# Kernel optimization log

Measured on AMD Instinct MI355X. Metric: run time of the kernel, lower is better.

The kernel has to match this reference:

```python
import jax, jax.numpy as jnp
import numpy as np

H = 8
DH = 64  # attention_head_size
HID = 512
NEG = -90000000000.0

def _lin(x, w, b):
    return x @ w + b

def _tfs(x):  # [N, HID] -> [H, N, DH]
    n = x.shape[0]
    return x.reshape(n, H, DH).transpose(1, 0, 2)

def _cross(q, ck, v, cv, mask, dw, db):
    # q: [H,N,DH], ck/cv: [H,M,DH], v: [H,N,DH], mask: [N,M]
    s = jnp.einsum('hnd,hmd->hnm', q, ck)
    s = s * mask[None, :, :] / jnp.sqrt(jnp.asarray(DH, s.dtype))
    s = jnp.where(s == 0.0, NEG, s)  # faithful zero->-inf hack
    p = jax.nn.softmax(s, axis=-1)
    ctx = v + jnp.einsum('hnm,hmd->hnd', p, cv)  # residual add of raw value
    n = ctx.shape[1]
    ctx = ctx.transpose(1, 0, 2).reshape(n, H * DH)
    return _lin(ctx, dw, db)

def setup_inputs() -> dict:
    key = jax.random.key(0)
    ks = jax.random.split(key, 24)
    N1, N2, D1 = 4096, 4096, 300
    d = {}
    d['h_head'] = jax.random.normal(ks[0], (N1, D1), jnp.float32)
    d['h_tail'] = jax.random.normal(ks[1], (N2, HID), jnp.float32)
    d['batch_head'] = jnp.sort(jax.random.randint(ks[2], (N1,), 0, 64))
    d['batch_tail'] = jnp.sort(jax.random.randint(ks[3], (N2,), 0, 64))
    def w(k, i, o):
        return jax.random.normal(k, (i, o), jnp.float32) / np.sqrt(i)
    d['map_w'] = w(ks[4], D1, HID); d['map_b'] = jnp.zeros((HID,), jnp.float32)
    names = ['q1', 'k1', 'v1', 'q2', 'k2', 'v2', 'd1', 'd2']
    for i, nm in enumerate(names):
        d[nm + '_w'] = w(ks[5 + i], HID, HID)
        d[nm + '_b'] = jnp.zeros((HID,), jnp.float32)
    return d

def reference(h_head, h_tail, batch_head, batch_tail,
              map_w, map_b,
              q1_w, q1_b, k1_w, k1_b, v1_w, v1_b,
              q2_w, q2_b, k2_w, k2_b, v2_w, v2_b,
              d1_w, d1_b, d2_w, d2_b):
    hh = _lin(h_head, map_w, map_b)  # n_dim1 != n_dim2 -> map
    q_h = _tfs(_lin(hh, q1_w, q1_b))
    k_h = _tfs(_lin(hh, k1_w, k1_b))
    v_h = _tfs(_lin(hh, v1_w, v1_b))
    q_t = _tfs(_lin(h_tail, q2_w, q2_b))
    k_t = _tfs(_lin(h_tail, k2_w, k2_b))
    v_t = _tfs(_lin(h_tail, v2_w, v2_b))
    mask = (batch_head[:, None] == batch_tail[None, :]).astype(jnp.float32)
    out_head = _cross(q_h, k_t, v_h, v_t, mask, d1_w, d1_b)
    out_tail = _cross(q_t, k_h, v_t, v_h, mask.T, d2_w, d2_b)
    return (out_head, out_tail)
```

## Files before the change

### kernel.cpp

```cpp
#include <hip/hip_runtime.h>
#include <hip/hip_bf16.h>
#include <math.h>


typedef __bf16 bf16x8 __attribute__((ext_vector_type(8)));
typedef float  f32x4  __attribute__((ext_vector_type(4)));

#define HID 512
#define NTOK 4096

#define AS1(p) ((const __attribute__((address_space(1))) void*)(p))
#define AS3(p) ((__attribute__((address_space(3))) void*)(p))

__global__ __launch_bounds__(256) void prep_inputs(
    const float* __restrict__ h_head, const float* __restrict__ h_tail,
    const int* __restrict__ bh, const int* __restrict__ bt,
    __bf16* __restrict__ hh_bf, __bf16* __restrict__ ht_bf,
    int* __restrict__ ranges)
{
    const int q = blockIdx.x, z = blockIdx.z, tid = threadIdx.x;

    if (z == 0) {
        if (q == 0 && tid < 128) {
            int b = tid & 63;
            const int* arr = (tid < 64) ? bh : bt;
            int base = (tid < 64) ? 0 : 128;
            int lo = 0, hi = NTOK;
            while (lo < hi) { int mid = (lo + hi) >> 1; if (arr[mid] < b) lo = mid + 1; else hi = mid; }
            int start = lo;
            lo = 0; hi = NTOK;
            while (lo < hi) { int mid = (lo + hi) >> 1; if (arr[mid] <= b) lo = mid + 1; else hi = mid; }
            ranges[base + b] = start;
            ranges[base + 64 + b] = lo;
        }
        for (int idx = tid; idx < 8 * 40; idx += 256) {
            int r   = q * 8 + idx / 40;
            int col = (idx % 40) * 8;
            bf16x8 v;
            if (col + 8 <= 300) {
                float4 f0 = *(const float4*)&h_head[(size_t)r * 300 + col];
                float4 f1 = *(const float4*)&h_head[(size_t)r * 300 + col + 4];
                v[0]=(__bf16)f0.x; v[1]=(__bf16)f0.y; v[2]=(__bf16)f0.z; v[3]=(__bf16)f0.w;
                v[4]=(__bf16)f1.x; v[5]=(__bf16)f1.y; v[6]=(__bf16)f1.z; v[7]=(__bf16)f1.w;
            } else if (col < 300) {
                float4 f0 = *(const float4*)&h_head[(size_t)r * 300 + col];
                v[0]=(__bf16)f0.x; v[1]=(__bf16)f0.y; v[2]=(__bf16)f0.z; v[3]=(__bf16)f0.w;
                v[4]=(__bf16)0.f; v[5]=(__bf16)0.f; v[6]=(__bf16)0.f; v[7]=(__bf16)0.f;
            } else {
                #pragma unroll
                for (int j = 0; j < 8; ++j) v[j] = (__bf16)0.f;
            }
            *(bf16x8*)&hh_bf[(size_t)r * 320 + col] = v;
        }
    } else {
        for (int idx = tid; idx < 8 * 64; idx += 256) {
            int r   = q * 8 + (idx >> 6);
            int col = (idx & 63) * 8;
            float4 f0 = *(const float4*)&h_tail[(size_t)r * 512 + col];
            float4 f1 = *(const float4*)&h_tail[(size_t)r * 512 + col + 4];
            bf16x8 v;
            v[0]=(__bf16)f0.x; v[1]=(__bf16)f0.y; v[2]=(__bf16)f0.z; v[3]=(__bf16)f0.w;
            v[4]=(__bf16)f1.x; v[5]=(__bf16)f1.y; v[6]=(__bf16)f1.z; v[7]=(__bf16)f1.w;
            *(bf16x8*)&ht_bf[(size_t)r * 512 + col] = v;
        }
    }
}

struct TransJobs {
    const float* src[9];
    __bf16*      dst[9];
    int          K[9];
    int          ldT[9];
};

__global__ __launch_bounds__(256) void transpose_weights(TransJobs tj) {
    const int z = blockIdx.z;
    const float* src = tj.src[z];
    __bf16* dst = tj.dst[z];
    const int K = tj.K[z], ldT = tj.ldT[z];
    const int tk = blockIdx.y * 64;
    const int tn = blockIdx.x * 64;
    if (tk >= ldT) return;

    __shared__ __bf16 T[64][72];
    const int tid = threadIdx.x;
    const int r0 = tid >> 4;
    const int c0 = (tid & 15) * 4;
    #pragma unroll
    for (int i = 0; i < 4; ++i) {
        int k = tk + r0 + i * 16;
        float4 v = (k < K) ? *(const float4*)&src[(size_t)k * 512 + tn + c0]
                           : float4{0.f, 0.f, 0.f, 0.f};
        T[r0 + i * 16][c0 + 0] = (__bf16)v.x;
        T[r0 + i * 16][c0 + 1] = (__bf16)v.y;
        T[r0 + i * 16][c0 + 2] = (__bf16)v.z;
        T[r0 + i * 16][c0 + 3] = (__bf16)v.w;
    }
    __syncthreads();

    const int n  = tid >> 2;
    const int kk = (tid & 3) * 16;
    bf16x8 o0, o1;
    #pragma unroll
    for (int j = 0; j < 8; ++j) { o0[j] = T[kk + j][n]; o1[j] = T[kk + 8 + j][n]; }
    __bf16* dp = dst + (size_t)(tn + n) * ldT + tk + kk;
    *(bf16x8*)dp       = o0;
    *(bf16x8*)(dp + 8) = o1;
}

struct GemmJobs {
    const __bf16* A[4];
    const __bf16* W[4];
    const float*  bias[4];
    void*         C[4];
    int           Kp[4];
};

template <typename TC>
__global__ __launch_bounds__(256) void gemm128(GemmJobs jobs) {
    __shared__ __align__(16) __bf16 As[2][4096];
    __shared__ __align__(16) __bf16 Bs[2][4096];

    const int z = blockIdx.z;
    const __bf16* A    = jobs.A[z];
    const __bf16* W    = jobs.W[z];
    const float*  bias = jobs.bias[z];
    TC*           C    = (TC*)jobs.C[z];
    const int     Kp   = jobs.Kp[z];

    const int tid  = threadIdx.x;
    const int wave = tid >> 6;
    const int lane = tid & 63;
    const int quad = lane >> 4;
    const int l16  = lane & 15;
    const int wy   = wave >> 1;
    const int wx   = wave & 1;
    const int rowBase = blockIdx.y * 128;
    const int colBase = blockIdx.x * 128;

    const int s_row = tid >> 2;
    const int s_kc  = ((tid & 3) ^ ((s_row >> 1) & 3)) * 8;

    const __bf16* gA = A + (size_t)(rowBase + s_row) * Kp + s_kc;
    const __bf16* gB = W + (size_t)(colBase + s_row) * Kp + s_kc;
    const int waveOff = wave * 512;

    f32x4 acc[4][4] = {};
    const int nk = Kp >> 5;

    __builtin_amdgcn_global_load_lds(AS1(gA),                   AS3(&As[0][waveOff]),        16, 0, 0);
    __builtin_amdgcn_global_load_lds(AS1(gA + (size_t)64 * Kp), AS3(&As[0][2048 + waveOff]), 16, 0, 0);
    __builtin_amdgcn_global_load_lds(AS1(gB),                   AS3(&Bs[0][waveOff]),        16, 0, 0);
    __builtin_amdgcn_global_load_lds(AS1(gB + (size_t)64 * Kp), AS3(&Bs[0][2048 + waveOff]), 16, 0, 0);

    for (int i = 0; i < nk; ++i) {
        const int cur = i & 1;
        __syncthreads();

        if (i + 1 < nk) {
            const int kt = (i + 1) * 32;
            const int nx = cur ^ 1;
            __builtin_amdgcn_global_load_lds(AS1(gA + kt),                   AS3(&As[nx][waveOff]),        16, 0, 0);
            __builtin_amdgcn_global_load_lds(AS1(gA + kt + (size_t)64 * Kp), AS3(&As[nx][2048 + waveOff]), 16, 0, 0);
            __builtin_amdgcn_global_load_lds(AS1(gB + kt),                   AS3(&Bs[nx][waveOff]),        16, 0, 0);
            __builtin_amdgcn_global_load_lds(AS1(gB + kt + (size_t)64 * Kp), AS3(&Bs[nx][2048 + waveOff]), 16, 0, 0);
        }

        bf16x8 ar[4], br[4];
        #pragma unroll
        for (int ii = 0; ii < 4; ++ii) {
            const int ra = wy * 64 + ii * 16 + l16;
            ar[ii] = *(const bf16x8*)&As[cur][ra * 32 + ((quad ^ ((ra >> 1) & 3)) << 3)];
        }
        #pragma unroll
        for (int jj = 0; jj < 4; ++jj) {
            const int rb = wx * 64 + jj * 16 + l16;
            br[jj] = *(const bf16x8*)&Bs[cur][rb * 32 + ((quad ^ ((rb >> 1) & 3)) << 3)];
        }
        #pragma unroll
        for (int ii = 0; ii < 4; ++ii)
            #pragma unroll
            for (int jj = 0; jj < 4; ++jj)
                acc[ii][jj] = __builtin_amdgcn_mfma_f32_16x16x32_bf16(ar[ii], br[jj], acc[ii][jj], 0, 0, 0);
    }

    #pragma unroll
    for (int jj = 0; jj < 4; ++jj) {
        int col = colBase + wx * 64 + jj * 16 + l16;
        float bv = bias[col];
        #pragma unroll
        for (int ii = 0; ii < 4; ++ii) {
            #pragma unroll
            for (int r = 0; r < 4; ++r) {
                int row = rowBase + wy * 64 + ii * 16 + quad * 4 + r;
                C[(size_t)row * HID + col] = (TC)(acc[ii][jj][r] + bv);
            }
        }
    }
}

__global__ __launch_bounds__(256) void attn_mfma(
    const __bf16* __restrict__ Q0, const __bf16* __restrict__ K0,
    const __bf16* __restrict__ Vr0, const __bf16* __restrict__ Vc0,
    const __bf16* __restrict__ Q1, const __bf16* __restrict__ K1,
    const __bf16* __restrict__ Vr1, const __bf16* __restrict__ Vc1,
    const int* __restrict__ ranges,
    __bf16* __restrict__ O0, __bf16* __restrict__ O1,
    int Nq, int Nk)
{
    __shared__ __align__(16) __bf16 Qs[64][72];
    __shared__ __align__(16) __bf16 Ks[64][72];
    __shared__ __align__(16) __bf16 Vt[64][72];
    __shared__ __align__(16) __bf16 Ps[64][72];

    const int z = blockIdx.z;
    const __bf16* Q    = z ? Q1 : Q0;
    const __bf16* Kg   = z ? K1 : K0;
    const __bf16* Vres = z ? Vr1 : Vr0;
    const __bf16* Vctx = z ? Vc1 : Vc0;
    __bf16* Out        = z ? O1 : O0;
    const int* qstart  = z ? ranges + 128 : ranges;
    const int* qend    = z ? ranges + 192 : ranges + 64;
    const int* kstart  = z ? ranges       : ranges + 128;
    const int* kend    = z ? ranges + 64  : ranges + 192;

    const int h = blockIdx.x, b = blockIdx.y;
    const int qs = qstart[b], qe = qend[b];
    const int ts = kstart[b], te = kend[b];
    const int nq = qe - qs, nk = te - ts;
    if (nq <= 0) return;

    const int tid  = threadIdx.x;
    const int wave = tid >> 6;
    const int lane = tid & 63;
    const int quad = lane >> 4;
    const int l16  = lane & 15;
    const int srow = tid >> 2;
    const int scol = (tid & 3) * 16;

    if (nk <= 0) {
        float* meanv = (float*)Qs;
        if (tid < 64) {
            float s = 0.f;
            for (int m = 0; m < Nk; ++m)
                s += (float)Vctx[(size_t)m * HID + h * 64 + tid];
            meanv[tid] = s / (float)Nk;
        }
        __syncthreads();
        int d = tid & 63;
        for (int r = qs + (tid >> 6); r < qe; r += 4) {
            size_t off = (size_t)r * HID + h * 64 + d;
            Out[off] = (__bf16)((float)Vres[off] + meanv[d]);
        }
        return;
    }

    for (int qc = 0; qc < nq; qc += 64) {
        __syncthreads();
        {
            int qg = min(qs + qc + srow, Nq - 1);
            const __bf16* src = Q + (size_t)qg * HID + h * 64 + scol;
            *(bf16x8*)&Qs[srow][scol]     = *(const bf16x8*)src;
            *(bf16x8*)&Qs[srow][scol + 8] = *(const bf16x8*)(src + 8);
        }
        __syncthreads();
        bf16x8 aq0 = *(const bf16x8*)&Qs[wave * 16 + l16][quad * 8];
        bf16x8 aq1 = *(const bf16x8*)&Qs[wave * 16 + l16][32 + quad * 8];

        f32x4 O[4] = {};
        float Mx[4], L[4];
        #pragma unroll
        for (int r = 0; r < 4; ++r) { Mx[r] = -__builtin_inff(); L[r] = 0.f; }

        for (int kc = 0; kc < nk; kc += 64) {
            __syncthreads();
            {
                int kg = min(ts + kc + srow, Nk - 1);
                const __bf16* ksrc = Kg + (size_t)kg * HID + h * 64 + scol;
                *(bf16x8*)&Ks[srow][scol]     = *(const bf16x8*)ksrc;
                *(bf16x8*)&Ks[srow][scol + 8] = *(const bf16x8*)(ksrc + 8);
                const __bf16* vsrc = Vctx + (size_t)kg * HID + h * 64 + scol;
                bf16x8 v0 = *(const bf16x8*)vsrc;
                bf16x8 v1 = *(const bf16x8*)(vsrc + 8);
                #pragma unroll
                for (int j = 0; j < 8; ++j) {
                    Vt[scol + j][srow]     = v0[j];
                    Vt[scol + 8 + j][srow] = v1[j];
                }
            }
            __syncthreads();

            f32x4 S[4] = {};
            #pragma unroll
            for (int c = 0; c < 4; ++c) {
                bf16x8 bk0 = *(const bf16x8*)&Ks[c * 16 + l16][quad * 8];
                bf16x8 bk1 = *(const bf16x8*)&Ks[c * 16 + l16][32 + quad * 8];
                S[c] = __builtin_amdgcn_mfma_f32_16x16x32_bf16(aq0, bk0, S[c], 0, 0, 0);
                S[c] = __builtin_amdgcn_mfma_f32_16x16x32_bf16(aq1, bk1, S[c], 0, 0, 0);
            }

            #pragma unroll
            for (int c = 0; c < 4; ++c) {
                bool valid = (ts + kc + c * 16 + l16) < te;
                #pragma unroll
                for (int r = 0; r < 4; ++r)
                    S[c][r] = valid ? S[c][r] * 0.125f : -__builtin_inff();
            }

            float cm[4], ps[4], alpha[4];
            #pragma unroll
            for (int r = 0; r < 4; ++r) {
                float v = fmaxf(fmaxf(S[0][r], S[1][r]), fmaxf(S[2][r], S[3][r]));
                v = fmaxf(v, __shfl_xor(v, 1, 64));
                v = fmaxf(v, __shfl_xor(v, 2, 64));
                v = fmaxf(v, __shfl_xor(v, 4, 64));
                v = fmaxf(v, __shfl_xor(v, 8, 64));
                cm[r] = v;
            }
            #pragma unroll
            for (int r = 0; r < 4; ++r) {
                float nM = fmaxf(Mx[r], cm[r]);
                alpha[r] = __expf(Mx[r] - nM);
                Mx[r] = nM;
                ps[r] = 0.f;
            }
            #pragma unroll
            for (int c = 0; c < 4; ++c)
                #pragma unroll
                for (int r = 0; r < 4; ++r) {
                    float p = __expf(S[c][r] - Mx[r]);
                    S[c][r] = p;
                    ps[r] += p;
                }
            #pragma unroll
            for (int r = 0; r < 4; ++r) {
                float v = ps[r];
                v += __shfl_xor(v, 1, 64);
                v += __shfl_xor(v, 2, 64);
                v += __shfl_xor(v, 4, 64);
                v += __shfl_xor(v, 8, 64);
                L[r] = L[r] * alpha[r] + v;
            }
            #pragma unroll
            for (int c = 0; c < 4; ++c)
                #pragma unroll
                for (int r = 0; r < 4; ++r)
                    O[c][r] *= alpha[r];

            #pragma unroll
            for (int c = 0; c < 4; ++c)
                #pragma unroll
                for (int r = 0; r < 4; ++r)
                    Ps[wave * 16 + quad * 4 + r][c * 16 + l16] = (__bf16)S[c][r];
            __syncthreads();

            bf16x8 ap0 = *(const bf16x8*)&Ps[wave * 16 + l16][quad * 8];
            bf16x8 ap1 = *(const bf16x8*)&Ps[wave * 16 + l16][32 + quad * 8];
            #pragma unroll
            for (int c = 0; c < 4; ++c) {
                bf16x8 bv0 = *(const bf16x8*)&Vt[c * 16 + l16][quad * 8];
                bf16x8 bv1 = *(const bf16x8*)&Vt[c * 16 + l16][32 + quad * 8];
                O[c] = __builtin_amdgcn_mfma_f32_16x16x32_bf16(ap0, bv0, O[c], 0, 0, 0);
                O[c] = __builtin_amdgcn_mfma_f32_16x16x32_bf16(ap1, bv1, O[c], 0, 0, 0);
            }
        }

        #pragma unroll
        for (int c = 0; c < 4; ++c) {
            int d = h * 64 + c * 16 + l16;
            #pragma unroll
            for (int r = 0; r < 4; ++r) {
                int qrow = qs + qc + wave * 16 + quad * 4 + r;
                if (qrow < qe) {
                    size_t off = (size_t)qrow * HID + d;
                    Out[off] = (__bf16)((float)Vres[off] + O[c][r] / L[r]);
                }
            }
        }
    }
}

extern "C" void kernel_launch(void* const* d_in, const int* in_sizes, int n_in,
                              void* d_out, int out_size, void* d_ws, size_t ws_size,
                              hipStream_t stream) {
    (void)in_sizes; (void)n_in; (void)out_size; (void)ws_size;

    const float* h_head = (const float*)d_in[0];
    const float* h_tail = (const float*)d_in[1];
    const int* batch_head = (const int*)d_in[2];
    const int* batch_tail = (const int*)d_in[3];
    const float* map_w = (const float*)d_in[4];
    const float* map_b = (const float*)d_in[5];
    const float* q1_w = (const float*)d_in[6];
    const float* q1_b = (const float*)d_in[7];
    const float* k1_w = (const float*)d_in[8];
    const float* k1_b = (const float*)d_in[9];
    const float* v1_w = (const float*)d_in[10];
    const float* v1_b = (const float*)d_in[11];
    const float* q2_w = (const float*)d_in[12];
    const float* q2_b = (const float*)d_in[13];
    const float* k2_w = (const float*)d_in[14];
    const float* k2_b = (const float*)d_in[15];
    const float* v2_w = (const float*)d_in[16];
    const float* v2_b = (const float*)d_in[17];
    const float* d1_w = (const float*)d_in[18];
    const float* d1_b = (const float*)d_in[19];
    const float* d2_w = (const float*)d_in[20];
    const float* d2_b = (const float*)d_in[21];

    float* out = (float*)d_out;

    const size_t SZ = (size_t)NTOK * HID;
    char* ws = (char*)d_ws;
    int* ranges = (int*)ws;
    __bf16* hh   = (__bf16*)(ws + 1024);
    __bf16* qh   = hh  + SZ;
    __bf16* kh   = qh  + SZ;
    __bf16* vh   = kh  + SZ;
    __bf16* qt   = vh  + SZ;
    __bf16* kt   = qt  + SZ;
    __bf16* vt   = kt  + SZ;
    __bf16* ctxh = vt  + SZ;
    __bf16* ctxt = ctxh + SZ;
    __bf16* mapT = ctxt + SZ;
    __bf16* q1T  = mapT + 512 * 320;
    __bf16* k1T  = q1T + 512 * 512;
    __bf16* v1T  = k1T + 512 * 512;
    __bf16* q2T  = v1T + 512 * 512;
    __bf16* k2T  = q2T + 512 * 512;
    __bf16* v2T  = k2T + 512 * 512;
    __bf16* d1T  = v2T + 512 * 512;
    __bf16* d2T  = d1T + 512 * 512;
    __bf16* hh_bf = d2T + 512 * 512;
    __bf16* ht_bf = hh_bf + (size_t)NTOK * 320;

    prep_inputs<<<dim3(512, 1, 2), dim3(256), 0, stream>>>(
        h_head, h_tail, batch_head, batch_tail, hh_bf, ht_bf, ranges);

    TransJobs tj;
    tj.src[0] = map_w; tj.dst[0] = mapT; tj.K[0] = 300; tj.ldT[0] = 320;
    const float* wsrc[8] = {q1_w, k1_w, v1_w, q2_w, k2_w, v2_w, d1_w, d2_w};
    __bf16* wdst[8] = {q1T, k1T, v1T, q2T, k2T, v2T, d1T, d2T};
    for (int i = 0; i < 8; ++i) {
        tj.src[i + 1] = wsrc[i]; tj.dst[i + 1] = wdst[i];
        tj.K[i + 1] = 512; tj.ldT[i + 1] = 512;
    }
    transpose_weights<<<dim3(8, 8, 9), dim3(256), 0, stream>>>(tj);

    {
        GemmJobs j;
        j.A[0] = hh_bf; j.W[0] = mapT; j.bias[0] = map_b; j.C[0] = hh; j.Kp[0] = 320;
        j.A[1] = ht_bf; j.W[1] = q2T; j.bias[1] = q2_b; j.C[1] = qt; j.Kp[1] = 512;
        j.A[2] = ht_bf; j.W[2] = k2T; j.bias[2] = k2_b; j.C[2] = kt; j.Kp[2] = 512;
        j.A[3] = ht_bf; j.W[3] = v2T; j.bias[3] = v2_b; j.C[3] = vt; j.Kp[3] = 512;
        gemm128<__bf16><<<dim3(4, 32, 4), dim3(256), 0, stream>>>(j);
    }
    {
        GemmJobs j;
        j.A[0] = hh; j.W[0] = q1T; j.bias[0] = q1_b; j.C[0] = qh; j.Kp[0] = 512;
        j.A[1] = hh; j.W[1] = k1T; j.bias[1] = k1_b; j.C[1] = kh; j.Kp[1] = 512;
        j.A[2] = hh; j.W[2] = v1T; j.bias[2] = v1_b; j.C[2] = vh; j.Kp[2] = 512;
        j.A[3] = hh; j.W[3] = v1T; j.bias[3] = v1_b; j.C[3] = vh; j.Kp[3] = 512;
        gemm128<__bf16><<<dim3(4, 32, 3), dim3(256), 0, stream>>>(j);
    }

    attn_mfma<<<dim3(8, 64, 2), dim3(256), 0, stream>>>(
        qh, kt, vh, vt,
        qt, kh, vt, vh,
        ranges, ctxh, ctxt, NTOK, NTOK);

    {
        GemmJobs j;
        j.A[0] = ctxh; j.W[0] = d1T; j.bias[0] = d1_b; j.C[0] = out;      j.Kp[0] = 512;
        j.A[1] = ctxt; j.W[1] = d2T; j.bias[1] = d2_b; j.C[1] = out + SZ; j.Kp[1] = 512;
        j.A[2] = ctxt; j.W[2] = d2T; j.bias[2] = d2_b; j.C[2] = out + SZ; j.Kp[2] = 512;
        j.A[3] = ctxt; j.W[3] = d2T; j.bias[3] = d2_b; j.C[3] = out + SZ; j.Kp[3] = 512;
        gemm128<float><<<dim3(4, 32, 2), dim3(256), 0, stream>>>(j);
    }
}
```

Baseline: 186.7 us.

## Fuse pipeline into one persistent cooperative kernel with grid syncs

Replaces the separate launches (input prep, weight transpose, two projection GEMM batches, attention, output GEMM) with a single persistent cooperative kernel. Each stage is distributed over blocks as work units and separated by grid-wide barriers, which removes per-launch overhead and inter-kernel gaps. GEMM tiles shrink from 128x128 to 64x128 to give more units and fit the shared-memory budget for four blocks per CU. The cost is grid-sync overhead, tail imbalance within each stage, and lower per-tile reuse in the GEMMs.

```diff
diff --git a/kernel.cpp b/kernel.cpp
--- a/kernel.cpp
+++ b/kernel.cpp
@@ -1,132 +1,43 @@
 #include <hip/hip_runtime.h>
+#include <hip/hip_cooperative_groups.h>
 #include <hip/hip_bf16.h>
 #include <math.h>
 
+namespace cg = cooperative_groups;
+
 
 typedef __bf16 bf16x8 __attribute__((ext_vector_type(8)));
 typedef float  f32x4  __attribute__((ext_vector_type(4)));
 
 #define HID 512
 #define NTOK 4096
+#define KHEAD 320
 
 #define AS1(p) ((const __attribute__((address_space(1))) void*)(p))
 #define AS3(p) ((__attribute__((address_space(3))) void*)(p))
 
-__global__ __launch_bounds__(256) void prep_inputs(
-    const float* __restrict__ h_head, const float* __restrict__ h_tail,
-    const int* __restrict__ bh, const int* __restrict__ bt,
-    __bf16* __restrict__ hh_bf, __bf16* __restrict__ ht_bf,
-    int* __restrict__ ranges)
+struct MegaArgs {
+    const float* h_head; const float* h_tail;
+    const int* bh; const int* bt;
+    const float* tsrc[9];
+    __bf16*      tdst[9];
+    __bf16* hh_bf; __bf16* ht_bf;
+    int* ranges;
+    const __bf16* g1A[4]; const __bf16* g1W[4]; const float* g1b[4]; __bf16* g1C[4]; int g1K[4];
+    const __bf16* g2A[3]; const __bf16* g2W[3]; const float* g2b[3]; __bf16* g2C[3];
+    const __bf16* qh; const __bf16* kh; const __bf16* vh;
+    const __bf16* qt; const __bf16* kt; const __bf16* vt;
+    __bf16* ctxh; __bf16* ctxt;
+    const __bf16* g4A[2]; const __bf16* g4W[2]; const float* g4b[2]; float* g4C[2];
+};
+
+template <typename TC>
+__device__ void gemm_unit(const __bf16* __restrict__ A, const __bf16* __restrict__ W,
+                          const float* __restrict__ bias, TC* __restrict__ C,
+                          int Kp, int bx, int by, char* smem)
 {
-    const int q = blockIdx.x, z = blockIdx.z, tid = threadIdx.x;
-
-    if (z == 0) {
-        if (q == 0 && tid < 128) {
-            int b = tid & 63;
-            const int* arr = (tid < 64) ? bh : bt;
-            int base = (tid < 64) ? 0 : 128;
-            int lo = 0, hi = NTOK;
-            while (lo < hi) { int mid = (lo + hi) >> 1; if (arr[mid] < b) lo = mid + 1; else hi = mid; }
-            int start = lo;
-            lo = 0; hi = NTOK;
-            while (lo < hi) { int mid = (lo + hi) >> 1; if (arr[mid] <= b) lo = mid + 1; else hi = mid; }
-            ranges[base + b] = start;
-            ranges[base + 64 + b] = lo;
-        }
-        for (int idx = tid; idx < 8 * 40; idx += 256) {
-            int r   = q * 8 + idx / 40;
-            int col = (idx % 40) * 8;
-            bf16x8 v;
-            if (col + 8 <= 300) {
-                float4 f0 = *(const float4*)&h_head[(size_t)r * 300 + col];
-                float4 f1 = *(const float4*)&h_head[(size_t)r * 300 + col + 4];
-                v[0]=(__bf16)f0.x; v[1]=(__bf16)f0.y; v[2]=(__bf16)f0.z; v[3]=(__bf16)f0.w;
-                v[4]=(__bf16)f1.x; v[5]=(__bf16)f1.y; v[6]=(__bf16)f1.z; v[7]=(__bf16)f1.w;
-            } else if (col < 300) {
-                float4 f0 = *(const float4*)&h_head[(size_t)r * 300 + col];
-                v[0]=(__bf16)f0.x; v[1]=(__bf16)f0.y; v[2]=(__bf16)f0.z; v[3]=(__bf16)f0.w;
-                v[4]=(__bf16)0.f; v[5]=(__bf16)0.f; v[6]=(__bf16)0.f; v[7]=(__bf16)0.f;
-            } else {
-                #pragma unroll
-                for (int j = 0; j < 8; ++j) v[j] = (__bf16)0.f;
-            }
-            *(bf16x8*)&hh_bf[(size_t)r * 320 + col] = v;
-        }
-    } else {
-        for (int idx = tid; idx < 8 * 64; idx += 256) {
-            int r   = q * 8 + (idx >> 6);
-            int col = (idx & 63) * 8;
-            float4 f0 = *(const float4*)&h_tail[(size_t)r * 512 + col];
-            float4 f1 = *(const float4*)&h_tail[(size_t)r * 512 + col + 4];
-            bf16x8 v;
-            v[0]=(__bf16)f0.x; v[1]=(__bf16)f0.y; v[2]=(__bf16)f0.z; v[3]=(__bf16)f0.w;
-            v[4]=(__bf16)f1.x; v[5]=(__bf16)f1.y; v[6]=(__bf16)f1.z; v[7]=(__bf16)f1.w;
-            *(bf16x8*)&ht_bf[(size_t)r * 512 + col] = v;
-        }
-    }
-}
-
-struct TransJobs {
-    const float* src[9];
-    __bf16*      dst[9];
-    int          K[9];
-    int          ldT[9];
-};
-
-__global__ __launch_bounds__(256) void transpose_weights(TransJobs tj) {
-    const int z = blockIdx.z;
-    const float* src = tj.src[z];
-    __bf16* dst = tj.dst[z];
-    const int K = tj.K[z], ldT = tj.ldT[z];
-    const int tk = blockIdx.y * 64;
-    const int tn = blockIdx.x * 64;
-    if (tk >= ldT) return;
-
-    __shared__ __bf16 T[64][72];
-    const int tid = threadIdx.x;
-    const int r0 = tid >> 4;
-    const int c0 = (tid & 15) * 4;
-    #pragma unroll
-    for (int i = 0; i < 4; ++i) {
-        int k = tk + r0 + i * 16;
-        float4 v = (k < K) ? *(const float4*)&src[(size_t)k * 512 + tn + c0]
-                           : float4{0.f, 0.f, 0.f, 0.f};
-        T[r0 + i * 16][c0 + 0] = (__bf16)v.x;
-        T[r0 + i * 16][c0 + 1] = (__bf16)v.y;
-        T[r0 + i * 16][c0 + 2] = (__bf16)v.z;
-        T[r0 + i * 16][c0 + 3] = (__bf16)v.w;
-    }
-    __syncthreads();
-
-    const int n  = tid >> 2;
-    const int kk = (tid & 3) * 16;
-    bf16x8 o0, o1;
-    #pragma unroll
-    for (int j = 0; j < 8; ++j) { o0[j] = T[kk + j][n]; o1[j] = T[kk + 8 + j][n]; }
-    __bf16* dp = dst + (size_t)(tn + n) * ldT + tk + kk;
-    *(bf16x8*)dp       = o0;
-    *(bf16x8*)(dp + 8) = o1;
-}
-
-struct GemmJobs {
-    const __bf16* A[4];
-    const __bf16* W[4];
-    const float*  bias[4];
-    void*         C[4];
-    int           Kp[4];
-};
-
-template <typename TC>
-__global__ __launch_bounds__(256) void gemm128(GemmJobs jobs) {
-    __shared__ __align__(16) __bf16 As[2][4096];
-    __shared__ __align__(16) __bf16 Bs[2][4096];
-
-    const int z = blockIdx.z;
-    const __bf16* A    = jobs.A[z];
-    const __bf16* W    = jobs.W[z];
-    const float*  bias = jobs.bias[z];
-    TC*           C    = (TC*)jobs.C[z];
-    const int     Kp   = jobs.Kp[z];
+    __bf16* As = (__bf16*)smem;
+    __bf16* Bs = (__bf16*)(smem + 8192);
 
     const int tid  = threadIdx.x;
     const int wave = tid >> 6;
@@ -135,8 +46,8 @@
     const int l16  = lane & 15;
     const int wy   = wave >> 1;
     const int wx   = wave & 1;
-    const int rowBase = blockIdx.y * 128;
-    const int colBase = blockIdx.x * 128;
+    const int rowBase = by * 64;
+    const int colBase = bx * 128;
 
     const int s_row = tid >> 2;
     const int s_kc  = ((tid & 3) ^ ((s_row >> 1) & 3)) * 8;
@@ -145,13 +56,13 @@
     const __bf16* gB = W + (size_t)(colBase + s_row) * Kp + s_kc;
     const int waveOff = wave * 512;
 
-    f32x4 acc[4][4] = {};
+    f32x4 acc[2][4] = {};
     const int nk = Kp >> 5;
 
-    __builtin_amdgcn_global_load_lds(AS1(gA),                   AS3(&As[0][waveOff]),        16, 0, 0);
-    __builtin_amdgcn_global_load_lds(AS1(gA + (size_t)64 * Kp), AS3(&As[0][2048 + waveOff]), 16, 0, 0);
-    __builtin_amdgcn_global_load_lds(AS1(gB),                   AS3(&Bs[0][waveOff]),        16, 0, 0);
-    __builtin_amdgcn_global_load_lds(AS1(gB + (size_t)64 * Kp), AS3(&Bs[0][2048 + waveOff]), 16, 0, 0);
+    __syncthreads();
+    __builtin_amdgcn_global_load_lds(AS1(gA),                   AS3(&As[waveOff]),        16, 0, 0);
+    __builtin_amdgcn_global_load_lds(AS1(gB),                   AS3(&Bs[waveOff]),        16, 0, 0);
+    __builtin_amdgcn_global_load_lds(AS1(gB + (size_t)64 * Kp), AS3(&Bs[2048 + waveOff]), 16, 0, 0);
 
     for (int i = 0; i < nk; ++i) {
         const int cur = i & 1;
@@ -160,25 +71,24 @@
         if (i + 1 < nk) {
             const int kt = (i + 1) * 32;
             const int nx = cur ^ 1;
-            __builtin_amdgcn_global_load_lds(AS1(gA + kt),                   AS3(&As[nx][waveOff]),        16, 0, 0);
-            __builtin_amdgcn_global_load_lds(AS1(gA + kt + (size_t)64 * Kp), AS3(&As[nx][2048 + waveOff]), 16, 0, 0);
-            __builtin_amdgcn_global_load_lds(AS1(gB + kt),                   AS3(&Bs[nx][waveOff]),        16, 0, 0);
-            __builtin_amdgcn_global_load_lds(AS1(gB + kt + (size_t)64 * Kp), AS3(&Bs[nx][2048 + waveOff]), 16, 0, 0);
-        }
-
-        bf16x8 ar[4], br[4];
-        #pragma unroll
-        for (int ii = 0; ii < 4; ++ii) {
-            const int ra = wy * 64 + ii * 16 + l16;
-            ar[ii] = *(const bf16x8*)&As[cur][ra * 32 + ((quad ^ ((ra >> 1) & 3)) << 3)];
+            __builtin_amdgcn_global_load_lds(AS1(gA + kt),                   AS3(&As[nx * 2048 + waveOff]),        16, 0, 0);
+            __builtin_amdgcn_global_load_lds(AS1(gB + kt),                   AS3(&Bs[nx * 4096 + waveOff]),        16, 0, 0);
+            __builtin_amdgcn_global_load_lds(AS1(gB + kt + (size_t)64 * Kp), AS3(&Bs[nx * 4096 + 2048 + waveOff]), 16, 0, 0);
+        }
+
+        bf16x8 ar[2], br[4];
+        #pragma unroll
+        for (int ii = 0; ii < 2; ++ii) {
+            const int ra = wy * 32 + ii * 16 + l16;
+            ar[ii] = *(const bf16x8*)&As[cur * 2048 + ra * 32 + ((quad ^ ((ra >> 1) & 3)) << 3)];
         }
         #pragma unroll
         for (int jj = 0; jj < 4; ++jj) {
             const int rb = wx * 64 + jj * 16 + l16;
-            br[jj] = *(const bf16x8*)&Bs[cur][rb * 32 + ((quad ^ ((rb >> 1) & 3)) << 3)];
-        }
-        #pragma unroll
-        for (int ii = 0; ii < 4; ++ii)
+            br[jj] = *(const bf16x8*)&Bs[cur * 4096 + rb * 32 + ((quad ^ ((rb >> 1) & 3)) << 3)];
+        }
+        #pragma unroll
+        for (int ii = 0; ii < 2; ++ii)
             #pragma unroll
             for (int jj = 0; jj < 4; ++jj)
                 acc[ii][jj] = __builtin_amdgcn_mfma_f32_16x16x32_bf16(ar[ii], br[jj], acc[ii][jj], 0, 0, 0);
@@ -189,42 +99,33 @@
         int col = colBase + wx * 64 + jj * 16 + l16;
         float bv = bias[col];
         #pragma unroll
-        for (int ii = 0; ii < 4; ++ii) {
+        for (int ii = 0; ii < 2; ++ii) {
             #pragma unroll
             for (int r = 0; r < 4; ++r) {
-                int row = rowBase + wy * 64 + ii * 16 + quad * 4 + r;
+                int row = rowBase + wy * 32 + ii * 16 + quad * 4 + r;
                 C[(size_t)row * HID + col] = (TC)(acc[ii][jj][r] + bv);
             }
         }
     }
 }
 
-__global__ __launch_bounds__(256) void attn_mfma(
-    const __bf16* __restrict__ Q0, const __bf16* __restrict__ K0,
-    const __bf16* __restrict__ Vr0, const __bf16* __restrict__ Vc0,
-    const __bf16* __restrict__ Q1, const __bf16* __restrict__ K1,
-    const __bf16* __restrict__ Vr1, const __bf16* __restrict__ Vc1,
-    const int* __restrict__ ranges,
-    __bf16* __restrict__ O0, __bf16* __restrict__ O1,
-    int Nq, int Nk)
+__device__ void attn_unit(const MegaArgs& a, int side, int h, int b, char* smem)
 {
-    __shared__ __align__(16) __bf16 Qs[64][72];
-    __shared__ __align__(16) __bf16 Ks[64][72];
-    __shared__ __align__(16) __bf16 Vt[64][72];
-    __shared__ __align__(16) __bf16 Ps[64][72];
-
-    const int z = blockIdx.z;
-    const __bf16* Q    = z ? Q1 : Q0;
-    const __bf16* Kg   = z ? K1 : K0;
-    const __bf16* Vres = z ? Vr1 : Vr0;
-    const __bf16* Vctx = z ? Vc1 : Vc0;
-    __bf16* Out        = z ? O1 : O0;
-    const int* qstart  = z ? ranges + 128 : ranges;
-    const int* qend    = z ? ranges + 192 : ranges + 64;
-    const int* kstart  = z ? ranges       : ranges + 128;
-    const int* kend    = z ? ranges + 64  : ranges + 192;
-
-    const int h = blockIdx.x, b = blockIdx.y;
+    __bf16 (*Qs)[72] = (__bf16(*)[72])(smem);
+    __bf16 (*Ks)[72] = (__bf16(*)[72])(smem + 9216);
+    __bf16 (*Vt)[72] = (__bf16(*)[72])(smem + 18432);
+    __bf16 (*Ps)[72] = (__bf16(*)[72])(smem + 27648);
+
+    const __bf16* Q    = side ? a.qt : a.qh;
+    const __bf16* Kg   = side ? a.kh : a.kt;
+    const __bf16* Vres = side ? a.vt : a.vh;
+    const __bf16* Vctx = side ? a.vh : a.vt;
+    __bf16* Out        = side ? a.ctxt : a.ctxh;
+    const int* qstart  = side ? a.ranges + 128 : a.ranges;
+    const int* qend    = side ? a.ranges + 192 : a.ranges + 64;
+    const int* kstart  = side ? a.ranges       : a.ranges + 128;
+    const int* kend    = side ? a.ranges + 64  : a.ranges + 192;
+
     const int qs = qstart[b], qe = qend[b];
     const int ts = kstart[b], te = kend[b];
     const int nq = qe - qs, nk = te - ts;
@@ -239,12 +140,13 @@
     const int scol = (tid & 3) * 16;
 
     if (nk <= 0) {
+        __syncthreads();
         float* meanv = (float*)Qs;
         if (tid < 64) {
             float s = 0.f;
-            for (int m = 0; m < Nk; ++m)
+            for (int m = 0; m < NTOK; ++m)
                 s += (float)Vctx[(size_t)m * HID + h * 64 + tid];
-            meanv[tid] = s / (float)Nk;
+            meanv[tid] = s / (float)NTOK;
         }
         __syncthreads();
         int d = tid & 63;
@@ -252,13 +154,14 @@
             size_t off = (size_t)r * HID + h * 64 + d;
             Out[off] = (__bf16)((float)Vres[off] + meanv[d]);
         }
+        __syncthreads();
         return;
     }
 
     for (int qc = 0; qc < nq; qc += 64) {
         __syncthreads();
         {
-            int qg = min(qs + qc + srow, Nq - 1);
+            int qg = min(qs + qc + srow, NTOK - 1);
             const __bf16* src = Q + (size_t)qg * HID + h * 64 + scol;
             *(bf16x8*)&Qs[srow][scol]     = *(const bf16x8*)src;
             *(bf16x8*)&Qs[srow][scol + 8] = *(const bf16x8*)(src + 8);
@@ -275,7 +178,7 @@
         for (int kc = 0; kc < nk; kc += 64) {
             __syncthreads();
             {
-                int kg = min(ts + kc + srow, Nk - 1);
+                int kg = min(ts + kc + srow, NTOK - 1);
                 const __bf16* ksrc = Kg + (size_t)kg * HID + h * 64 + scol;
                 *(bf16x8*)&Ks[srow][scol]     = *(const bf16x8*)ksrc;
                 *(bf16x8*)&Ks[srow][scol + 8] = *(const bf16x8*)(ksrc + 8);
@@ -377,6 +280,129 @@
                 }
             }
         }
+    }
+}
+
+__global__ __launch_bounds__(256, 4) void mega(MegaArgs a)
+{
+    __shared__ __align__(16) char smem[36864];
+    cg::grid_group grid = cg::this_grid();
+    const int tid = threadIdx.x;
+    const int NB  = gridDim.x;
+
+    for (int u = blockIdx.x; u < 1600; u += NB) {
+        if (u < 512) {
+            if (u == 0 && tid < 128) {
+                int b = tid & 63;
+                const int* arr = (tid < 64) ? a.bh : a.bt;
+                int base = (tid < 64) ? 0 : 128;
+                int lo = 0, hi = NTOK;
+                while (lo < hi) { int mid = (lo + hi) >> 1; if (arr[mid] < b) lo = mid + 1; else hi = mid; }
+                int start = lo;
+                lo = 0; hi = NTOK;
+                while (lo < hi) { int mid = (lo + hi) >> 1; if (arr[mid] <= b) lo = mid + 1; else hi = mid; }
+                a.ranges[base + b] = start;
+                a.ranges[base + 64 + b] = lo;
+            }
+            for (int idx = tid; idx < 8 * 40; idx += 256) {
+                int r   = u * 8 + idx / 40;
+                int col = (idx % 40) * 8;
+                bf16x8 v;
+                if (col + 8 <= 300) {
+                    float4 f0 = *(const float4*)&a.h_head[(size_t)r * 300 + col];
+                    float4 f1 = *(const float4*)&a.h_head[(size_t)r * 300 + col + 4];
+                    v[0]=(__bf16)f0.x; v[1]=(__bf16)f0.y; v[2]=(__bf16)f0.z; v[3]=(__bf16)f0.w;
+                    v[4]=(__bf16)f1.x; v[5]=(__bf16)f1.y; v[6]=(__bf16)f1.z; v[7]=(__bf16)f1.w;
+                } else if (col < 300) {
+                    float4 f0 = *(const float4*)&a.h_head[(size_t)r * 300 + col];
+                    v[0]=(__bf16)f0.x; v[1]=(__bf16)f0.y; v[2]=(__bf16)f0.z; v[3]=(__bf16)f0.w;
+                    v[4]=(__bf16)0.f; v[5]=(__bf16)0.f; v[6]=(__bf16)0.f; v[7]=(__bf16)0.f;
+                } else {
+                    #pragma unroll
+                    for (int j = 0; j < 8; ++j) v[j] = (__bf16)0.f;
+                }
+                *(bf16x8*)&a.hh_bf[(size_t)r * KHEAD + col] = v;
+            }
+        } else if (u < 1024) {
+            int q = u - 512;
+            for (int idx = tid; idx < 8 * 64; idx += 256) {
+                int r   = q * 8 + (idx >> 6);
+                int col = (idx & 63) * 8;
+                float4 f0 = *(const float4*)&a.h_tail[(size_t)r * 512 + col];
+                float4 f1 = *(const float4*)&a.h_tail[(size_t)r * 512 + col + 4];
+                bf16x8 v;
+                v[0]=(__bf16)f0.x; v[1]=(__bf16)f0.y; v[2]=(__bf16)f0.z; v[3]=(__bf16)f0.w;
+                v[4]=(__bf16)f1.x; v[5]=(__bf16)f1.y; v[6]=(__bf16)f1.z; v[7]=(__bf16)f1.w;
+                *(bf16x8*)&a.ht_bf[(size_t)r * 512 + col] = v;
+            }
+        } else {
+            int t  = u - 1024;
+            int w  = t >> 6;
+            int j2 = t & 63;
+            int tn = (j2 & 7) * 64;
+            int tk = (j2 >> 3) * 64;
+            const int K   = (w == 0) ? 300 : 512;
+            const int ldT = (w == 0) ? KHEAD : 512;
+            if (tk < ldT) {
+                __bf16 (*T)[72] = (__bf16(*)[72])smem;
+                __syncthreads();
+                const float* src = a.tsrc[w];
+                __bf16* dst = a.tdst[w];
+                const int r0 = tid >> 4;
+                const int c0 = (tid & 15) * 4;
+                #pragma unroll
+                for (int i = 0; i < 4; ++i) {
+                    int k = tk + r0 + i * 16;
+                    float4 v = (k < K) ? *(const float4*)&src[(size_t)k * 512 + tn + c0]
+                                       : float4{0.f, 0.f, 0.f, 0.f};
+                    T[r0 + i * 16][c0 + 0] = (__bf16)v.x;
+                    T[r0 + i * 16][c0 + 1] = (__bf16)v.y;
+                    T[r0 + i * 16][c0 + 2] = (__bf16)v.z;
+                    T[r0 + i * 16][c0 + 3] = (__bf16)v.w;
+                }
+                __syncthreads();
+                const int n  = tid >> 2;
+                const int kk = (tid & 3) * 16;
+                bf16x8 o0, o1;
+                #pragma unroll
+                for (int j = 0; j < 8; ++j) { o0[j] = T[kk + j][n]; o1[j] = T[kk + 8 + j][n]; }
+                __bf16* dp = dst + (size_t)(tn + n) * ldT + tk + kk;
+                *(bf16x8*)dp       = o0;
+                *(bf16x8*)(dp + 8) = o1;
+            }
+        }
+    }
+    __threadfence();
+    grid.sync();
+
+    for (int u = blockIdx.x; u < 1024; u += NB) {
+        int z = u >> 8, t = u & 255;
+        gemm_unit<__bf16>(a.g1A[z], a.g1W[z], a.g1b[z], a.g1C[z], a.g1K[z],
+                          t & 3, t >> 2, smem);
+    }
+    __threadfence();
+    grid.sync();
+
+    for (int u = blockIdx.x; u < 768; u += NB) {
+        int z = u >> 8, t = u & 255;
+        gemm_unit<__bf16>(a.g2A[z], a.g2W[z], a.g2b[z], a.g2C[z], 512,
+                          t & 3, t >> 2, smem);
+    }
+    __threadfence();
+    grid.sync();
+
+    for (int u = blockIdx.x; u < 1024; u += NB) {
+        int side = u >> 9;
+        int rem  = u & 511;
+        attn_unit(a, side, rem & 7, rem >> 3, smem);
+    }
+    __threadfence();
+    grid.sync();
+
+    for (int u = blockIdx.x; u < 512; u += NB) {
+        int z = u >> 8, t = u & 255;
+        gemm_unit<float>(a.g4A[z], a.g4W[z], a.g4b[z], a.g4C[z], 512,
+                         t & 3, t >> 2, smem);
     }
 }
 
@@ -423,7 +449,7 @@
     __bf16* ctxh = vt  + SZ;
     __bf16* ctxt = ctxh + SZ;
     __bf16* mapT = ctxt + SZ;
-    __bf16* q1T  = mapT + 512 * 320;
+    __bf16* q1T  = mapT + 512 * KHEAD;
     __bf16* k1T  = q1T + 512 * 512;
     __bf16* v1T  = k1T + 512 * 512;
     __bf16* q2T  = v1T + 512 * 512;
@@ -432,49 +458,39 @@
     __bf16* d1T  = v2T + 512 * 512;
     __bf16* d2T  = d1T + 512 * 512;
     __bf16* hh_bf = d2T + 512 * 512;
-    __bf16* ht_bf = hh_bf + (size_t)NTOK * 320;
-
-    prep_inputs<<<dim3(512, 1, 2), dim3(256), 0, stream>>>(
-        h_head, h_tail, batch_head, batch_tail, hh_bf, ht_bf, ranges);
-
-    TransJobs tj;
-    tj.src[0] = map_w; tj.dst[0] = mapT; tj.K[0] = 300; tj.ldT[0] = 320;
+    __bf16* ht_bf = hh_bf + (size_t)NTOK * KHEAD;
+
+    MegaArgs ma;
+    ma.h_head = h_head; ma.h_tail = h_tail; ma.bh = batch_head; ma.bt = batch_tail;
+    ma.tsrc[0] = map_w; ma.tdst[0] = mapT;
     const float* wsrc[8] = {q1_w, k1_w, v1_w, q2_w, k2_w, v2_w, d1_w, d2_w};
     __bf16* wdst[8] = {q1T, k1T, v1T, q2T, k2T, v2T, d1T, d2T};
-    for (int i = 0; i < 8; ++i) {
-        tj.src[i + 1] = wsrc[i]; tj.dst[i + 1] = wdst[i];
-        tj.K[i + 1] = 512; tj.ldT[i + 1] = 512;
-    }
-    transpose_weights<<<dim3(8, 8, 9), dim3(256), 0, stream>>>(tj);
-
-    {
-        GemmJobs j;
-        j.A[0] = hh_bf; j.W[0] = mapT; j.bias[0] = map_b; j.C[0] = hh; j.Kp[0] = 320;
-        j.A[1] = ht_bf; j.W[1] = q2T; j.bias[1] = q2_b; j.C[1] = qt; j.Kp[1] = 512;
-        j.A[2] = ht_bf; j.W[2] = k2T; j.bias[2] = k2_b; j.C[2] = kt; j.Kp[2] = 512;
-        j.A[3] = ht_bf; j.W[3] = v2T; j.bias[3] = v2_b; j.C[3] = vt; j.Kp[3] = 512;
-        gemm128<__bf16><<<dim3(4, 32, 4), dim3(256), 0, stream>>>(j);
-    }
-    {
-        GemmJobs j;
-        j.A[0] = hh; j.W[0] = q1T; j.bias[0] = q1_b; j.C[0] = qh; j.Kp[0] = 512;
-        j.A[1] = hh; j.W[1] = k1T; j.bias[1] = k1_b; j.C[1] = kh; j.Kp[1] = 512;
-        j.A[2] = hh; j.W[2] = v1T; j.bias[2] = v1_b; j.C[2] = vh; j.Kp[2] = 512;
-        j.A[3] = hh; j.W[3] = v1T; j.bias[3] = v1_b; j.C[3] = vh; j.Kp[3] = 512;
-        gemm128<__bf16><<<dim3(4, 32, 3), dim3(256), 0, stream>>>(j);
-    }
-
-    attn_mfma<<<dim3(8, 64, 2), dim3(256), 0, stream>>>(
-        qh, kt, vh, vt,
-        qt, kh, vt, vh,
-        ranges, ctxh, ctxt, NTOK, NTOK);
-
-    {
-        GemmJobs j;
-        j.A[0] = ctxh; j.W[0] = d1T; j.bias[0] = d1_b; j.C[0] = out;      j.Kp[0] = 512;
-        j.A[1] = ctxt; j.W[1] = d2T; j.bias[1] = d2_b; j.C[1] = out + SZ; j.Kp[1] = 512;
-        j.A[2] = ctxt; j.W[2] = d2T; j.bias[2] = d2_b; j.C[2] = out + SZ; j.Kp[2] = 512;
-        j.A[3] = ctxt; j.W[3] = d2T; j.bias[3] = d2_b; j.C[3] = out + SZ; j.Kp[3] = 512;
-        gemm128<float><<<dim3(4, 32, 2), dim3(256), 0, stream>>>(j);
-    }
+    for (int i = 0; i < 8; ++i) { ma.tsrc[i + 1] = wsrc[i]; ma.tdst[i + 1] = wdst[i]; }
+    ma.hh_bf = hh_bf; ma.ht_bf = ht_bf; ma.ranges = ranges;
+
+    ma.g1A[0] = hh_bf; ma.g1W[0] = mapT; ma.g1b[0] = map_b; ma.g1C[0] = hh; ma.g1K[0] = KHEAD;
+    ma.g1A[1] = ht_bf; ma.g1W[1] = q2T;  ma.g1b[1] = q2_b;  ma.g1C[1] = qt; ma.g1K[1] = 512;
+    ma.g1A[2] = ht_bf; ma.g1W[2] = k2T;  ma.g1b[2] = k2_b;  ma.g1C[2] = kt; ma.g1K[2] = 512;
+    ma.g1A[3] = ht_bf; ma.g1W[3] = v2T;  ma.g1b[3] = v2_b;  ma.g1C[3] = vt; ma.g1K[3] = 512;
+
+    ma.g2A[0] = hh; ma.g2W[0] = q1T; ma.g2b[0] = q1_b; ma.g2C[0] = qh;
+    ma.g2A[1] = hh; ma.g2W[1] = k1T; ma.g2b[1] = k1_b; ma.g2C[1] = kh;
+    ma.g2A[2] = hh; ma.g2W[2] = v1T; ma.g2b[2] = v1_b; ma.g2C[2] = vh;
+
+    ma.qh = qh; ma.kh = kh; ma.vh = vh;
+    ma.qt = qt; ma.kt = kt; ma.vt = vt;
+    ma.ctxh = ctxh; ma.ctxt = ctxt;
+
+    ma.g4A[0] = ctxh; ma.g4W[0] = d1T; ma.g4b[0] = d1_b; ma.g4C[0] = out;
+    ma.g4A[1] = ctxt; ma.g4W[1] = d2T; ma.g4b[1] = d2_b; ma.g4C[1] = out + SZ;
+
+    int perCU = 0;
+    hipError_t oe = hipOccupancyMaxActiveBlocksPerMultiprocessor(&perCU, mega, 256, 0);
+    if (oe != hipSuccess || perCU <= 0) perCU = 2;
+    if (perCU > 4) perCU = 4;
+    int NB = perCU * 256;
+    if (NB > 1024) NB = 1024;
+
+    void* kp[] = { (void*)&ma };
+    hipLaunchCooperativeKernel((const void*)mega, dim3(NB), dim3(256), kp, 0, stream);
 }
```

Measured after the change: 679.9 us. 264% more time.
